# Optimization experiments

Hardware: AMD Instinct MI355X
Metric: run time of the kernel (lower is better)

The kernel has to match this reference:

```python
import jax, jax.numpy as jnp
import numpy as np

F_IN, F_H, N_A, N_B = 256, 512, 40, 4
N_GRAPHS, NODES_PER_GRAPH = 4096, 32
N_NODES = N_GRAPHS * NODES_PER_GRAPH
D_OUT = N_B + N_B * N_A  # 164
BN_EPS = 1e-5


def setup_inputs() -> dict:
    key = jax.random.key(0)
    ks = jax.random.split(key, 8)
    X = jax.random.normal(ks[0], (N_NODES, F_IN), dtype=jnp.float32)
    # fixed-size graphs: consistent NX / NX_rep pair
    NX = jnp.full((N_GRAPHS,), NODES_PER_GRAPH, dtype=jnp.int64)
    NX_rep = jnp.repeat(jnp.arange(N_GRAPHS, dtype=jnp.int64), NODES_PER_GRAPH)
    def kaiming(k, fo, fi):
        return jax.random.normal(k, (fo, fi), dtype=jnp.float32) * np.float32(1.0 / np.sqrt(fi))
    return {
        "X": X, "NX": NX, "NX_rep": NX_rep,
        "W_h": kaiming(ks[1], F_H, 2 * F_IN),          # linear_h (no bias)
        "g_h": jnp.ones((F_H,), jnp.float32), "b_h": jnp.zeros((F_H,), jnp.float32),
        "W_ht": kaiming(ks[2], F_H, F_IN),              # linear_h_t (no bias)
        "g_ht": jnp.ones((F_H,), jnp.float32), "b_ht": jnp.zeros((F_H,), jnp.float32),
        "W_x": kaiming(ks[3], D_OUT, F_H) * 0.1,        # linear_x
        "b_x": jnp.zeros((D_OUT,), jnp.float32),
        "W_xt": kaiming(ks[4], 1, F_H) * 0.1,           # linear_x_t
        "b_xt": jnp.zeros((1,), jnp.float32),
    }


def _batchnorm(x, gamma, beta):
    # BatchNorm1d in training mode: batch statistics, biased variance
    mean = jnp.mean(x, axis=0)
    var = jnp.var(x, axis=0)
    return (x - mean) * jax.lax.rsqrt(var + BN_EPS) * gamma + beta


def reference(X, NX, NX_rep, W_h, g_h, b_h, W_ht, g_ht, b_ht, W_x, b_x, W_xt, b_xt):
    n_graphs = NX.shape[0]
    # graph-level mean pooling via segment sum  -> [G, F_in]
    X_end = jax.ops.segment_sum(X, NX_rep, num_segments=n_graphs) / NX[:, None].astype(X.dtype)
    # concat node features with gathered graph context -> [N, 2*F_in]
    Xc = jnp.concatenate([X, X_end[NX_rep]], axis=1)
    X_h = jax.nn.relu(_batchnorm(Xc @ W_h.T, g_h, b_h))          # [N, F_h]
    X_h_end = jax.nn.relu(_batchnorm(X_end @ W_ht.T, g_ht, b_ht))  # [G, F_h]
    X_x = jnp.exp(X_h @ W_x.T + b_x)                              # [N, D_OUT]
    X_x_end = jnp.exp(X_h_end @ W_xt.T + b_xt)                    # [G, 1]
    # segmented softmax denominator (per graph, over all nodes x D_OUT + end logit)
    X_sum = jnp.sum(jax.ops.segment_sum(X_x, NX_rep, num_segments=n_graphs),
                    axis=-1, keepdims=True) + X_x_end             # [G, 1]
    X_softmax = X_x / X_sum[NX_rep]                               # [N, D_OUT]
    X_softmax_end = X_x_end / X_sum                               # [G, 1]
    connect = X_softmax[:, :N_B]                                  # [N, N_B]
    append = X_softmax[:, N_B:].reshape(-1, N_A, N_B)             # [N, N_A, N_B]
    end = X_softmax_end.squeeze(-1)                               # [G]
    return (append, connect, end)
```

## Files before the change

kernel.cpp:

```cpp
#include <hip/hip_runtime.h>
#include <hip/hip_bf16.h>

typedef __hip_bfloat16 bf16;
typedef __attribute__((ext_vector_type(8))) short bf16x8;
typedef __attribute__((ext_vector_type(4))) float f32x4;

#define N_NODES   131072
#define N_GRAPHS  4096
#define FIN       256
#define FH        512
#define NPAD      176
#define NREAL     164

#define OFF_XB     0UL
#define OFF_XENDB  67108864UL
#define OFF_W1A    69206016UL
#define OFF_BCAT   69468160UL
#define OFF_WXB    69992448UL
#define OFF_STATS  70172672UL
#define OFF_XXE    70180864UL
#define OFF_CCAT   70197248UL
#define OFF_H      86974464UL

__device__ __forceinline__ void gld_lds16(const void* g, void* l) {
  __builtin_amdgcn_global_load_lds(
      (const __attribute__((address_space(1))) void*)g,
      (__attribute__((address_space(3))) void*)l, 16, 0, 0);
}

__device__ __forceinline__ float bf2f(unsigned short u) {
  unsigned int x = ((unsigned int)u) << 16; float f;
  __builtin_memcpy(&f, &x, 4); return f;
}
__device__ __forceinline__ unsigned short f2bf(float f) {
  bf16 h = __float2bfloat16(f); unsigned short u;
  __builtin_memcpy(&u, &h, 2); return u;
}

__global__ __launch_bounds__(256) void k_wcast(
    const float* __restrict__ W_h, const float* __restrict__ W_ht,
    const float* __restrict__ W_x,
    bf16* __restrict__ W1a, bf16* __restrict__ Bcat, bf16* __restrict__ Wxb,
    float* __restrict__ stats)
{
  int i = blockIdx.x * 256 + threadIdx.x;
  if (i < 2048) stats[i] = 0.f;
  if (i < 512 * 512) {
    int of = i >> 9, ic = i & 511;
    float v = W_h[i];
    if (ic < 256) W1a[of * 256 + ic] = __float2bfloat16(v);
    else          Bcat[of * 256 + (ic - 256)] = __float2bfloat16(v);
  }
  if (i < 512 * 256) Bcat[512 * 256 + i] = __float2bfloat16(W_ht[i]);
  if (i < NPAD * 512) {
    int n = i >> 9;
    Wxb[i] = (n < NREAL) ? __float2bfloat16(W_x[i]) : __float2bfloat16(0.f);
  }
}

__global__ __launch_bounds__(256) void k_xend(
    const float* __restrict__ X, const int* __restrict__ NX,
    bf16* __restrict__ Xb, bf16* __restrict__ X_endb)
{
  int g = blockIdx.x;
  int t = threadIdx.x;
  int cg = t & 63;
  int rg = t >> 6;
  const float* Xg = X + (long)g * 32 * FIN;
  bf16* Xbg = Xb + (long)g * 32 * FIN;
  float4 s = {0.f, 0.f, 0.f, 0.f};
  #pragma unroll
  for (int r = 0; r < 8; ++r) {
    int off = (rg * 8 + r) * FIN + cg * 4;
    float4 v = *(const float4*)(Xg + off);
    s.x += v.x; s.y += v.y; s.z += v.z; s.w += v.w;
    ushort4 u = {f2bf(v.x), f2bf(v.y), f2bf(v.z), f2bf(v.w)};
    *(ushort4*)(Xbg + off) = u;
  }
  __shared__ float4 red[256];
  red[t] = s;
  __syncthreads();
  if (t < 64) {
    float4 a = red[t], b = red[t + 64], c = red[t + 128], d = red[t + 192];
    float inv = 1.f / (float)NX[g];
    float4 m = {(a.x + b.x + c.x + d.x) * inv, (a.y + b.y + c.y + d.y) * inv,
                (a.z + b.z + c.z + d.z) * inv, (a.w + b.w + c.w + d.w) * inv};
    ushort4 u = {f2bf(m.x), f2bf(m.y), f2bf(m.z), f2bf(m.w)};
    *(ushort4*)(X_endb + (long)g * FIN + t * 4) = u;
  }
}

__global__ __launch_bounds__(256, 2) void gemm0(
    const bf16* __restrict__ A, const bf16* __restrict__ B,
    float* __restrict__ Cout, float* __restrict__ s1e, float* __restrict__ s2e)
{
  const int bid = blockIdx.x;
  const int blkM = bid >> 3, blkN = bid & 7;
  const int tid = threadIdx.x;
  const int w = tid >> 6, lane = tid & 63;
  const int wm = w >> 1, wn = w & 1;

  __shared__ __align__(16) bf16 lA[128 * 32];
  __shared__ __align__(16) bf16 lB[128 * 32];
  __shared__ float sred[2][2][128];

  f32x4 acc[4][4] = {};
  const int rS = lane >> 2;
  const int cS = (lane & 3) * 8;
  const long baseA = (long)blkM * 128;
  const long baseB = (long)blkN * 128;

  for (int kk = 0; kk < FIN; kk += 32) {
    #pragma unroll
    for (int c = 0; c < 2; ++c) {
      int chunk = 2 * w + c;
      gld_lds16(A + (baseA + chunk * 16 + rS) * FIN + kk + cS, &lA[chunk * 16 * 32]);
      gld_lds16(B + (baseB + chunk * 16 + rS) * FIN + kk + cS, &lB[chunk * 16 * 32]);
    }
    __syncthreads();
    bf16x8 a8[4], b8[4];
    #pragma unroll
    for (int t = 0; t < 4; ++t) {
      a8[t] = *(const bf16x8*)&lA[(wm * 64 + t * 16 + (lane & 15)) * 32 + (lane >> 4) * 8];
      b8[t] = *(const bf16x8*)&lB[(wn * 64 + t * 16 + (lane & 15)) * 32 + (lane >> 4) * 8];
    }
    #pragma unroll
    for (int tm = 0; tm < 4; ++tm)
      #pragma unroll
      for (int tn = 0; tn < 4; ++tn)
        acc[tm][tn] = __builtin_amdgcn_mfma_f32_16x16x32_bf16(a8[tm], b8[tn], acc[tm][tn], 0, 0, 0);
    __syncthreads();
  }

  const int rowq = (lane >> 4) * 4;
  const int coll = lane & 15;
  float p1[4] = {0.f, 0.f, 0.f, 0.f}, p2[4] = {0.f, 0.f, 0.f, 0.f};
  #pragma unroll
  for (int tm = 0; tm < 4; ++tm)
    #pragma unroll
    for (int tn = 0; tn < 4; ++tn)
      #pragma unroll
      for (int r = 0; r < 4; ++r) {
        long row = baseA + wm * 64 + tm * 16 + rowq + r;
        int col = (int)baseB + wn * 64 + tn * 16 + coll;
        float v = acc[tm][tn][r];
        Cout[row * 1024 + col] = v;
        p1[tn] += v; p2[tn] += v * v;
      }

  if (blkN >= 4) {
    #pragma unroll
    for (int tn = 0; tn < 4; ++tn) {
      float q1 = p1[tn], q2 = p2[tn];
      q1 += __shfl_xor(q1, 16); q1 += __shfl_xor(q1, 32);
      q2 += __shfl_xor(q2, 16); q2 += __shfl_xor(q2, 32);
      if (lane < 16) {
        sred[wm][0][wn * 64 + tn * 16 + lane] = q1;
        sred[wm][1][wn * 64 + tn * 16 + lane] = q2;
      }
    }
    __syncthreads();
    int st = tid >> 7, c = tid & 127;
    float v = sred[0][st][c] + sred[1][st][c];
    atomicAdd((st ? s2e : s1e) + (blkN - 4) * 128 + c, v);
  }
}

__global__ __launch_bounds__(256) void k_xxend(
    const float* __restrict__ Ccat, const float* __restrict__ s1e,
    const float* __restrict__ s2e, const float* __restrict__ g_ht,
    const float* __restrict__ b_ht, const float* __restrict__ Wxt,
    const float* __restrict__ bxt, float* __restrict__ Xxe)
{
  __shared__ float aL[512], cL[512];
  int tid = threadIdx.x;
  #pragma unroll
  for (int i = tid; i < 512; i += 256) {
    float mean = s1e[i] * 2.44140625e-4f;
    float var = s2e[i] * 2.44140625e-4f - mean * mean;
    float a = g_ht[i] / sqrtf(var + 1e-5f);
    aL[i] = a; cL[i] = b_ht[i] - mean * a;
  }
  __syncthreads();
  int w = tid >> 6, lane = tid & 63;
  int g = blockIdx.x * 4 + w;
  const float* h = Ccat + (long)g * 1024 + 512;
  float acc = 0.f;
  #pragma unroll
  for (int i = 0; i < 8; ++i) {
    int j = lane + i * 64;
    float x = fmaxf(aL[j] * h[j] + cL[j], 0.f);
    acc += x * Wxt[j];
  }
  #pragma unroll
  for (int off = 32; off; off >>= 1) acc += __shfl_xor(acc, off);
  if (lane == 0) Xxe[g] = expf(acc + bxt[0]);
}

__global__ __launch_bounds__(512) void gemm1(
    const bf16* __restrict__ Xb, const bf16* __restrict__ W1a,
    const float* __restrict__ Ccat, bf16* __restrict__ H,
    float* __restrict__ s1m, float* __restrict__ s2m)
{
  const int bid = blockIdx.x;
  const int tid = threadIdx.x;
  const int w = tid >> 6, lane = tid & 63;
  const int rS = lane >> 2;
  const int cS = (lane & 3) * 8;
  const int hi = lane >> 4;
  const int coll = lane & 15;

  __shared__ __align__(16) bf16 ring[8][4][2048];

  bf16x8 b8[4][8];
  #pragma unroll
  for (int j = 0; j < 4; ++j)
    #pragma unroll
    for (int ks = 0; ks < 8; ++ks)
      b8[j][ks] = *(const bf16x8*)(W1a + (w * 64 + j * 16 + coll) * FIN
                                   + ks * 32 + hi * 8);

  const long rowbase = (long)bid * 512;
  #pragma unroll
  for (int s = 0; s < 2; ++s)
    #pragma unroll
    for (int c = 0; c < 4; ++c)
      gld_lds16(Xb + (rowbase + c * 16 + rS) * FIN + s * 32 + cS,
                &ring[w][s][c * 512]);

  f32x4 acc[4][4] = {};
  float p1[4] = {0.f, 0.f, 0.f, 0.f}, p2[4] = {0.f, 0.f, 0.f, 0.f};

  #pragma unroll 1
  for (int mt = 0; mt < 8; ++mt) {
    const long g0 = (rowbase >> 5) + mt * 2;
    float ct[2][4];
    #pragma unroll
    for (int a = 0; a < 2; ++a)
      #pragma unroll
      for (int j = 0; j < 4; ++j)
        ct[a][j] = Ccat[(g0 + a) * 1024 + w * 64 + j * 16 + coll];

    #pragma unroll
    for (int ks = 0; ks < 8; ++ks) {
      if (ks < 2) asm volatile("s_waitcnt vmcnt(12)" ::: "memory");
      else        asm volatile("s_waitcnt vmcnt(4)" ::: "memory");

      {
        int tgt = mt * 8 + ks + 2; if (tgt > 63) tgt = 63;
        const bf16* src = Xb + (rowbase + (long)(tgt >> 3) * 64 + rS) * FIN
                          + (tgt & 7) * 32 + cS;
        #pragma unroll
        for (int c = 0; c < 4; ++c)
          gld_lds16(src + c * 16 * FIN, &ring[w][(ks + 2) & 3][c * 512]);
      }

      bf16x8 a8[4];
      #pragma unroll
      for (int t = 0; t < 4; ++t)
        a8[t] = *(const bf16x8*)&ring[w][ks & 3][(t * 16 + coll) * 32 + hi * 8];
      #pragma unroll
      for (int t = 0; t < 4; ++t)
        #pragma unroll
        for (int j = 0; j < 4; ++j)
          acc[t][j] = __builtin_amdgcn_mfma_f32_16x16x32_bf16(
              a8[t], b8[j][ks], acc[t][j], 0, 0, 0);
    }

    const long rtile = rowbase + (long)mt * 64;
    #pragma unroll
    for (int t = 0; t < 4; ++t)
      #pragma unroll
      for (int j = 0; j < 4; ++j) {
        int col = w * 64 + j * 16 + coll;
        #pragma unroll
        for (int r = 0; r < 4; ++r) {
          float h = acc[t][j][r] + ct[t >> 1][j];
          H[(rtile + t * 16 + hi * 4 + r) * FH + col] = __float2bfloat16(h);
          p1[j] += h; p2[j] += h * h;
        }
        acc[t][j][0] = 0.f; acc[t][j][1] = 0.f;
        acc[t][j][2] = 0.f; acc[t][j][3] = 0.f;
      }
  }

  #pragma unroll
  for (int j = 0; j < 4; ++j) {
    float q1 = p1[j], q2 = p2[j];
    q1 += __shfl_xor(q1, 16); q1 += __shfl_xor(q1, 32);
    q2 += __shfl_xor(q2, 16); q2 += __shfl_xor(q2, 32);
    if (lane < 16) {
      atomicAdd(s1m + w * 64 + j * 16 + lane, q1);
      atomicAdd(s2m + w * 64 + j * 16 + lane, q2);
    }
  }
}

__global__ __launch_bounds__(256, 2) void gemm2(
    const bf16* __restrict__ Hraw, const bf16* __restrict__ Wxb,
    const float* __restrict__ s1m, const float* __restrict__ s2m,
    const float* __restrict__ g_h, const float* __restrict__ b_h,
    const float* __restrict__ b_x, const float* __restrict__ Xxe,
    float* __restrict__ outA, float* __restrict__ outC, float* __restrict__ outE)
{
  const int blk = blockIdx.x;
  const int tid = threadIdx.x;
  const int w = tid >> 6, lane = tid & 63;

  __shared__ __align__(16) bf16 lA[128 * 32];
  __shared__ __align__(16) bf16 lB[NPAD * 32];
  __shared__ float aL[512], cL[512];

  #pragma unroll
  for (int i = tid; i < 512; i += 256) {
    float mean = s1m[i] * 7.62939453125e-6f;
    float var = s2m[i] * 7.62939453125e-6f - mean * mean;
    float a = g_h[i] / sqrtf(var + 1e-5f);
    aL[i] = a; cL[i] = b_h[i] - mean * a;
  }
  __syncthreads();

  f32x4 acc[2][11] = {};
  const int rS = lane >> 2;
  const int cS = (lane & 3) * 8;
  const long baseRow = (long)blk * 128;

  for (int kk = 0; kk < FH; kk += 32) {
    for (int o = w; o < 11; o += 4)
      gld_lds16(Wxb + (o * 16 + rS) * FH + kk + cS, &lB[o * 16 * 32]);

    f32x4 a0 = *(const f32x4*)&aL[kk + cS];
    f32x4 a1 = *(const f32x4*)&aL[kk + cS + 4];
    f32x4 c0 = *(const f32x4*)&cL[kk + cS];
    f32x4 c1 = *(const f32x4*)&cL[kk + cS + 4];
    #pragma unroll
    for (int c = 0; c < 2; ++c) {
      int chunk = 2 * w + c;
      uint4 raw = *(const uint4*)(Hraw + (baseRow + chunk * 16 + rS) * FH + kk + cS);
      unsigned short* u = (unsigned short*)&raw;
      #pragma unroll
      for (int j = 0; j < 4; ++j) {
        float v = bf2f(u[j]);
        u[j] = f2bf(fmaxf(a0[j] * v + c0[j], 0.f));
      }
      #pragma unroll
      for (int j = 0; j < 4; ++j) {
        float v = bf2f(u[4 + j]);
        u[4 + j] = f2bf(fmaxf(a1[j] * v + c1[j], 0.f));
      }
      *(uint4*)&lA[(chunk * 16 + rS) * 32 + cS] = raw;
    }
    __syncthreads();

    bf16x8 a8[2], b8[11];
    #pragma unroll
    for (int t = 0; t < 2; ++t)
      a8[t] = *(const bf16x8*)&lA[(w * 32 + t * 16 + (lane & 15)) * 32 + (lane >> 4) * 8];
    #pragma unroll
    for (int t = 0; t < 11; ++t)
      b8[t] = *(const bf16x8*)&lB[(t * 16 + (lane & 15)) * 32 + (lane >> 4) * 8];
    #pragma unroll
    for (int tm = 0; tm < 2; ++tm)
      #pragma unroll
      for (int tn = 0; tn < 11; ++tn)
        acc[tm][tn] = __builtin_amdgcn_mfma_f32_16x16x32_bf16(a8[tm], b8[tn], acc[tm][tn], 0, 0, 0);
    __syncthreads();
  }

  const int rowq = (lane >> 4) * 4;
  const int coll = lane & 15;
  const int g = blk * 4 + w;
  float psum = 0.f;
  #pragma unroll
  for (int tn = 0; tn < 11; ++tn) {
    int col = tn * 16 + coll;
    bool valid = col < NREAL;
    float bx = valid ? b_x[col] : 0.f;
    #pragma unroll
    for (int tm = 0; tm < 2; ++tm)
      #pragma unroll
      for (int r = 0; r < 4; ++r) {
        float p = valid ? expf(acc[tm][tn][r] + bx) : 0.f;
        acc[tm][tn][r] = p;
        psum += p;
      }
  }
  #pragma unroll
  for (int off = 32; off; off >>= 1) psum += __shfl_xor(psum, off);
  float Xe = Xxe[g];
  float inv = 1.0f / (psum + Xe);
  if (lane == 0) outE[g] = Xe * inv;

  #pragma unroll
  for (int tn = 0; tn < 11; ++tn) {
    int col = tn * 16 + coll;
    if (col >= NREAL) continue;
    #pragma unroll
    for (int tm = 0; tm < 2; ++tm)
      #pragma unroll
      for (int r = 0; r < 4; ++r) {
        long row = baseRow + w * 32 + tm * 16 + rowq + r;
        float v = acc[tm][tn][r] * inv;
        if (col >= 4) outA[row * 160 + (col - 4)] = v;
        else          outC[row * 4 + col] = v;
      }
  }
}

extern "C" void kernel_launch(void* const* d_in, const int* in_sizes, int n_in,
                              void* d_out, int out_size, void* d_ws, size_t ws_size,
                              hipStream_t stream)
{
  const float* X    = (const float*)d_in[0];
  const int*   NX   = (const int*)d_in[1];
  const float* W_h  = (const float*)d_in[3];
  const float* g_h  = (const float*)d_in[4];
  const float* b_h  = (const float*)d_in[5];
  const float* W_ht = (const float*)d_in[6];
  const float* g_ht = (const float*)d_in[7];
  const float* b_ht = (const float*)d_in[8];
  const float* W_x  = (const float*)d_in[9];
  const float* b_x  = (const float*)d_in[10];
  const float* W_xt = (const float*)d_in[11];
  const float* b_xt = (const float*)d_in[12];

  char* ws = (char*)d_ws;
  bf16*  Xb    = (bf16*)(ws + OFF_XB);
  bf16*  X_endb= (bf16*)(ws + OFF_XENDB);
  bf16*  W1a   = (bf16*)(ws + OFF_W1A);
  bf16*  Bcat  = (bf16*)(ws + OFF_BCAT);
  bf16*  Wxb   = (bf16*)(ws + OFF_WXB);
  float* stats = (float*)(ws + OFF_STATS);
  float* s1m = stats, *s2m = stats + 512, *s1e = stats + 1024, *s2e = stats + 1536;
  float* Xxe   = (float*)(ws + OFF_XXE);
  float* Ccat  = (float*)(ws + OFF_CCAT);
  bf16*  H     = (bf16*)(ws + OFF_H);

  float* outA = (float*)d_out;
  float* outC = outA + (long)N_NODES * 160;
  float* outE = outC + (long)N_NODES * 4;

  k_wcast<<<1024, 256, 0, stream>>>(W_h, W_ht, W_x, W1a, Bcat, Wxb, stats);
  k_xend<<<N_GRAPHS, 256, 0, stream>>>(X, NX, Xb, X_endb);
  gemm0<<<256, 256, 0, stream>>>(X_endb, Bcat, Ccat, s1e, s2e);
  k_xxend<<<1024, 256, 0, stream>>>(Ccat, s1e, s2e, g_ht, b_ht, W_xt, b_xt, Xxe);
  gemm1<<<256, 512, 0, stream>>>(Xb, W1a, Ccat, H, s1m, s2m);
  gemm2<<<1024, 256, 0, stream>>>(H, Wxb, s1m, s2m, g_h, b_h, b_x, Xxe, outA, outC, outE);
}
```

Baseline: 389.8 us.

## Deepen gemm1 prefetch pipeline, defer H stores, and drop block syncs in gemm2

In gemm1 the X prefetch ring moves from two stages ahead to three. The bf16 H stores for each 64-row tile are packed into registers and spread across the MFMA steps of the next tile, with the vmcnt waits retuned to count those stores. In gemm2 each wave now owns its own LDS A tile, the next K-slice of H is prefetched into registers, and the W_x fragments are read straight from global memory. That removes both per-iteration __syncthreads and the shared B staging. The cost is more registers in gemm1, the loss of the occupancy hint on gemm2, and repeated global reads of W_x by every wave.

New measurement: 479.8 us. 23.1% more time.

```diff
diff --git a/kernel.cpp b/kernel.cpp
--- a/kernel.cpp
+++ b/kernel.cpp
@@ -197,6 +197,74 @@
   if (lane == 0) Xxe[g] = expf(acc + bxt[0]);
 }
 
+#define G1WAIT(WN) asm volatile("s_waitcnt vmcnt(" #WN ")" ::: "memory");
+
+#define G1S(MTV, KS, WN, DOST)                                                 \
+  {                                                                            \
+    G1WAIT(WN)                                                                 \
+    if ((KS) == 0) {                                                           \
+      long g0_ = ((long)(MTV)) * 2 + (rowbase >> 5);                           \
+      _Pragma("unroll")                                                        \
+      for (int a_ = 0; a_ < 2; ++a_)                                           \
+        _Pragma("unroll")                                                      \
+        for (int j_ = 0; j_ < 4; ++j_)                                         \
+          ct[a_][j_] = Ccat[(g0_ + a_) * 1024 + w * 64 + j_ * 16 + coll];      \
+    }                                                                          \
+    { int tgt_ = (MTV) * 8 + (KS) + 3; if (tgt_ > 63) tgt_ = 63;               \
+      const bf16* src_ = Xb + (rowbase + (long)(tgt_ >> 3) * 64 + rS) * FIN    \
+                         + (tgt_ & 7) * 32 + cS;                               \
+      _Pragma("unroll")                                                        \
+      for (int c_ = 0; c_ < 4; ++c_)                                           \
+        gld_lds16(src_ + c_ * 16 * FIN, &ring[w][((KS) + 3) & 3][c_ * 512]); } \
+    bf16x8 a8_[4];                                                             \
+    _Pragma("unroll")                                                          \
+    for (int t_ = 0; t_ < 4; ++t_)                                             \
+      a8_[t_] = *(const bf16x8*)&ring[w][(KS) & 3][(t_ * 16 + coll) * 32       \
+                                                   + hi * 8];                  \
+    _Pragma("unroll")                                                          \
+    for (int t_ = 0; t_ < 4; ++t_)                                             \
+      _Pragma("unroll")                                                        \
+      for (int j_ = 0; j_ < 4; ++j_)                                           \
+        acc[t_][j_] = __builtin_amdgcn_mfma_f32_16x16x32_bf16(                 \
+            a8_[t_], b8[j_][KS], acc[t_][j_], 0, 0, 0);                        \
+    if (DOST) {                                                                \
+      const int t_ = (KS) >> 1;                                                \
+      long rp_ = rowbase + (long)((MTV) - 1) * 64 + t_ * 16 + hi * 4;          \
+      _Pragma("unroll")                                                        \
+      for (int jj_ = 0; jj_ < 2; ++jj_) {                                      \
+        const int j_ = ((KS) & 1) * 2 + jj_;                                   \
+        _Pragma("unroll")                                                      \
+        for (int rr_ = 0; rr_ < 2; ++rr_) {                                    \
+          unsigned pk_ = hold[t_ * 8 + j_ * 2 + rr_];                          \
+          bf16* p_ = H + (rp_ + rr_ * 2) * FH + w * 64 + j_ * 16 + coll;       \
+          *(unsigned short*)p_ = (unsigned short)(pk_ & 0xffff);               \
+          *(unsigned short*)(p_ + FH) = (unsigned short)(pk_ >> 16);           \
+        }                                                                      \
+      }                                                                        \
+    }                                                                          \
+  }
+
+#define G1CONV()                                                               \
+  {                                                                            \
+    _Pragma("unroll")                                                          \
+    for (int t_ = 0; t_ < 4; ++t_)                                             \
+      _Pragma("unroll")                                                        \
+      for (int j_ = 0; j_ < 4; ++j_) {                                         \
+        float h0_ = acc[t_][j_][0] + ct[t_ >> 1][j_];                          \
+        float h1_ = acc[t_][j_][1] + ct[t_ >> 1][j_];                          \
+        float h2_ = acc[t_][j_][2] + ct[t_ >> 1][j_];                          \
+        float h3_ = acc[t_][j_][3] + ct[t_ >> 1][j_];                          \
+        p1[j_] += h0_ + h1_ + h2_ + h3_;                                       \
+        p2[j_] += h0_ * h0_ + h1_ * h1_ + h2_ * h2_ + h3_ * h3_;               \
+        hold[t_ * 8 + j_ * 2 + 0] =                                            \
+            (unsigned)f2bf(h0_) | ((unsigned)f2bf(h1_) << 16);                 \
+        hold[t_ * 8 + j_ * 2 + 1] =                                            \
+            (unsigned)f2bf(h2_) | ((unsigned)f2bf(h3_) << 16);                 \
+        acc[t_][j_][0] = 0.f; acc[t_][j_][1] = 0.f;                            \
+        acc[t_][j_][2] = 0.f; acc[t_][j_][3] = 0.f;                            \
+      }                                                                        \
+  }
+
 __global__ __launch_bounds__(512) void gemm1(
     const bf16* __restrict__ Xb, const bf16* __restrict__ W1a,
     const float* __restrict__ Ccat, bf16* __restrict__ H,
@@ -222,7 +290,7 @@
 
   const long rowbase = (long)bid * 512;
   #pragma unroll
-  for (int s = 0; s < 2; ++s)
+  for (int s = 0; s < 3; ++s)
     #pragma unroll
     for (int c = 0; c < 4; ++c)
       gld_lds16(Xb + (rowbase + c * 16 + rS) * FIN + s * 32 + cS,
@@ -230,59 +298,34 @@
 
   f32x4 acc[4][4] = {};
   float p1[4] = {0.f, 0.f, 0.f, 0.f}, p2[4] = {0.f, 0.f, 0.f, 0.f};
-
+  float ct[2][4];
+  unsigned hold[32];
+
+  G1S(0, 0, 8, 0) G1S(0, 1, 8, 0) G1S(0, 2, 8, 0) G1S(0, 3, 8, 0)
+  G1S(0, 4, 8, 0) G1S(0, 5, 8, 0) G1S(0, 6, 8, 0) G1S(0, 7, 8, 0)
+  G1CONV()
+  G1S(1, 0, 8, 1)  G1S(1, 1, 16, 1) G1S(1, 2, 24, 1) G1S(1, 3, 32, 1)
+  G1S(1, 4, 32, 1) G1S(1, 5, 32, 1) G1S(1, 6, 32, 1) G1S(1, 7, 32, 1)
+  G1CONV()
   #pragma unroll 1
-  for (int mt = 0; mt < 8; ++mt) {
-    const long g0 = (rowbase >> 5) + mt * 2;
-    float ct[2][4];
-    #pragma unroll
-    for (int a = 0; a < 2; ++a)
-      #pragma unroll
-      for (int j = 0; j < 4; ++j)
-        ct[a][j] = Ccat[(g0 + a) * 1024 + w * 64 + j * 16 + coll];
-
-    #pragma unroll
-    for (int ks = 0; ks < 8; ++ks) {
-      if (ks < 2) asm volatile("s_waitcnt vmcnt(12)" ::: "memory");
-      else        asm volatile("s_waitcnt vmcnt(4)" ::: "memory");
-
-      {
-        int tgt = mt * 8 + ks + 2; if (tgt > 63) tgt = 63;
-        const bf16* src = Xb + (rowbase + (long)(tgt >> 3) * 64 + rS) * FIN
-                          + (tgt & 7) * 32 + cS;
-        #pragma unroll
-        for (int c = 0; c < 4; ++c)
-          gld_lds16(src + c * 16 * FIN, &ring[w][(ks + 2) & 3][c * 512]);
-      }
-
-      bf16x8 a8[4];
-      #pragma unroll
-      for (int t = 0; t < 4; ++t)
-        a8[t] = *(const bf16x8*)&ring[w][ks & 3][(t * 16 + coll) * 32 + hi * 8];
-      #pragma unroll
-      for (int t = 0; t < 4; ++t)
-        #pragma unroll
-        for (int j = 0; j < 4; ++j)
-          acc[t][j] = __builtin_amdgcn_mfma_f32_16x16x32_bf16(
-              a8[t], b8[j][ks], acc[t][j], 0, 0, 0);
-    }
-
-    const long rtile = rowbase + (long)mt * 64;
-    #pragma unroll
-    for (int t = 0; t < 4; ++t)
-      #pragma unroll
-      for (int j = 0; j < 4; ++j) {
-        int col = w * 64 + j * 16 + coll;
-        #pragma unroll
-        for (int r = 0; r < 4; ++r) {
-          float h = acc[t][j][r] + ct[t >> 1][j];
-          H[(rtile + t * 16 + hi * 4 + r) * FH + col] = __float2bfloat16(h);
-          p1[j] += h; p2[j] += h * h;
-        }
-        acc[t][j][0] = 0.f; acc[t][j][1] = 0.f;
-        acc[t][j][2] = 0.f; acc[t][j][3] = 0.f;
-      }
-  }
+  for (int mt = 2; mt < 8; ++mt) {
+    G1S(mt, 0, 32, 1) G1S(mt, 1, 32, 1) G1S(mt, 2, 32, 1) G1S(mt, 3, 32, 1)
+    G1S(mt, 4, 32, 1) G1S(mt, 5, 32, 1) G1S(mt, 6, 32, 1) G1S(mt, 7, 32, 1)
+    G1CONV()
+  }
+
+  #pragma unroll
+  for (int t = 0; t < 4; ++t)
+    #pragma unroll
+    for (int j = 0; j < 4; ++j)
+      #pragma unroll
+      for (int rr = 0; rr < 2; ++rr) {
+        unsigned pk = hold[t * 8 + j * 2 + rr];
+        bf16* p = H + (rowbase + 7 * 64 + t * 16 + hi * 4 + rr * 2) * FH
+                  + w * 64 + j * 16 + coll;
+        *(unsigned short*)p = (unsigned short)(pk & 0xffff);
+        *(unsigned short*)(p + FH) = (unsigned short)(pk >> 16);
+      }
 
   #pragma unroll
   for (int j = 0; j < 4; ++j) {
@@ -296,7 +339,7 @@
   }
 }
 
-__global__ __launch_bounds__(256, 2) void gemm2(
+__global__ __launch_bounds__(256) void gemm2(
     const bf16* __restrict__ Hraw, const bf16* __restrict__ Wxb,
     const float* __restrict__ s1m, const float* __restrict__ s2m,
     const float* __restrict__ g_h, const float* __restrict__ b_h,
@@ -306,9 +349,12 @@
   const int blk = blockIdx.x;
   const int tid = threadIdx.x;
   const int w = tid >> 6, lane = tid & 63;
-
-  __shared__ __align__(16) bf16 lA[128 * 32];
-  __shared__ __align__(16) bf16 lB[NPAD * 32];
+  const int rS = lane >> 2;
+  const int cS = (lane & 3) * 8;
+  const int hi = lane >> 4;
+  const int coll = lane & 15;
+
+  __shared__ __align__(16) bf16 lA[4][32 * 32];
   __shared__ float aL[512], cL[512];
 
   #pragma unroll
@@ -320,55 +366,76 @@
   }
   __syncthreads();
 
+  const long baseRow = (long)blk * 128;
+  const long wrow = baseRow + w * 32;
+
+  #define G2X(rawv, kof)                                                     \
+    { f32x4 a0_ = *(const f32x4*)&aL[(kof) + cS];                            \
+      f32x4 a1_ = *(const f32x4*)&aL[(kof) + cS + 4];                        \
+      f32x4 c0_ = *(const f32x4*)&cL[(kof) + cS];                            \
+      f32x4 c1_ = *(const f32x4*)&cL[(kof) + cS + 4];                        \
+      unsigned short* u_ = (unsigned short*)&(rawv);                         \
+      _Pragma("unroll")                                                      \
+      for (int q_ = 0; q_ < 4; ++q_) {                                       \
+        float v_ = bf2f(u_[q_]);                                             \
+        u_[q_] = f2bf(fmaxf(a0_[q_] * v_ + c0_[q_], 0.f));                   \
+      }                                                                      \
+      _Pragma("unroll")                                                      \
+      for (int q_ = 0; q_ < 4; ++q_) {                                       \
+        float v_ = bf2f(u_[4 + q_]);                                         \
+        u_[4 + q_] = f2bf(fmaxf(a1_[q_] * v_ + c1_[q_], 0.f));               \
+      }                                                                      \
+    }
+
+  uint4 hreg[2];
+  #pragma unroll
+  for (int c = 0; c < 2; ++c) {
+    uint4 raw = *(const uint4*)(Hraw + (wrow + c * 16 + rS) * FH + cS);
+    G2X(raw, 0)
+    *(uint4*)&lA[w][(c * 16 + rS) * 32 + cS] = raw;
+  }
+  #pragma unroll
+  for (int c = 0; c < 2; ++c)
+    hreg[c] = *(const uint4*)(Hraw + (wrow + c * 16 + rS) * FH + 32 + cS);
+
   f32x4 acc[2][11] = {};
-  const int rS = lane >> 2;
-  const int cS = (lane & 3) * 8;
-  const long baseRow = (long)blk * 128;
-
+
+  #pragma unroll 1
   for (int kk = 0; kk < FH; kk += 32) {
-    for (int o = w; o < 11; o += 4)
-      gld_lds16(Wxb + (o * 16 + rS) * FH + kk + cS, &lB[o * 16 * 32]);
-
-    f32x4 a0 = *(const f32x4*)&aL[kk + cS];
-    f32x4 a1 = *(const f32x4*)&aL[kk + cS + 4];
-    f32x4 c0 = *(const f32x4*)&cL[kk + cS];
-    f32x4 c1 = *(const f32x4*)&cL[kk + cS + 4];
-    #pragma unroll
-    for (int c = 0; c < 2; ++c) {
-      int chunk = 2 * w + c;
-      uint4 raw = *(const uint4*)(Hraw + (baseRow + chunk * 16 + rS) * FH + kk + cS);
-      unsigned short* u = (unsigned short*)&raw;
-      #pragma unroll
-      for (int j = 0; j < 4; ++j) {
-        float v = bf2f(u[j]);
-        u[j] = f2bf(fmaxf(a0[j] * v + c0[j], 0.f));
-      }
-      #pragma unroll
-      for (int j = 0; j < 4; ++j) {
-        float v = bf2f(u[4 + j]);
-        u[4 + j] = f2bf(fmaxf(a1[j] * v + c1[j], 0.f));
-      }
-      *(uint4*)&lA[(chunk * 16 + rS) * 32 + cS] = raw;
+    bf16x8 a8[2];
+    #pragma unroll
+    for (int t = 0; t < 2; ++t)
+      a8[t] = *(const bf16x8*)&lA[w][(t * 16 + coll) * 32 + hi * 8];
+
+    if (kk + 32 < FH) {
+      #pragma unroll
+      for (int c = 0; c < 2; ++c) {
+        uint4 raw = hreg[c];
+        G2X(raw, kk + 32)
+        *(uint4*)&lA[w][(c * 16 + rS) * 32 + cS] = raw;
+      }
+      if (kk + 64 < FH) {
+        #pragma unroll
+        for (int c = 0; c < 2; ++c)
+          hreg[c] = *(const uint4*)(Hraw + (wrow + c * 16 + rS) * FH
+                                    + kk + 64 + cS);
+      }
     }
-    __syncthreads();
-
-    bf16x8 a8[2], b8[11];
-    #pragma unroll
-    for (int t = 0; t < 2; ++t)
-      a8[t] = *(const bf16x8*)&lA[(w * 32 + t * 16 + (lane & 15)) * 32 + (lane >> 4) * 8];
-    #pragma unroll
-    for (int t = 0; t < 11; ++t)
-      b8[t] = *(const bf16x8*)&lB[(t * 16 + (lane & 15)) * 32 + (lane >> 4) * 8];
+
+    bf16x8 bb[11];
+    #pragma unroll
+    for (int o = 0; o < 11; ++o)
+      bb[o] = *(const bf16x8*)(Wxb + (o * 16 + coll) * FH + kk + hi * 8);
+
     #pragma unroll
     for (int tm = 0; tm < 2; ++tm)
       #pragma unroll
       for (int tn = 0; tn < 11; ++tn)
-        acc[tm][tn] = __builtin_amdgcn_mfma_f32_16x16x32_bf16(a8[tm], b8[tn], acc[tm][tn], 0, 0, 0);
-    __syncthreads();
-  }
-
-  const int rowq = (lane >> 4) * 4;
-  const int coll = lane & 15;
+        acc[tm][tn] = __builtin_amdgcn_mfma_f32_16x16x32_bf16(
+            a8[tm], bb[tn], acc[tm][tn], 0, 0, 0);
+  }
+
+  const int rowq = hi * 4;
   const int g = blk * 4 + w;
   float psum = 0.f;
   #pragma unroll
```
